# Performance work log

Measured on AMD Instinct MI355X. Metric: run time of the kernel, lower is better.

Reference implementation:

```python
import jax, jax.numpy as jnp
import numpy as np

B, N, DIN, DMID, DOUT, E = 64, 5000, 64, 128, 32, 80000


def setup_inputs() -> dict:
    key = jax.random.key(0)
    ks = jax.random.split(key, 12)
    p = lambda k, shape: jax.random.normal(k, shape, jnp.float32) * 0.05
    return {
        "x": jax.random.normal(ks[0], (B, N, DIN), jnp.float32),
        "edge_index": jax.random.randint(ks[1], (2, E), 0, N),
        "prev_hidden_state": jax.random.normal(ks[2], (B, N, DMID), jnp.float32),
        # GCNConv weights/biases for gates z, r, h
        "Wg_z": p(ks[3], (DIN, DMID)), "bg_z": jnp.zeros((DMID,), jnp.float32),
        "Wg_r": p(ks[4], (DIN, DMID)), "bg_r": jnp.zeros((DMID,), jnp.float32),
        "Wg_h": p(ks[5], (DIN, DMID)), "bg_h": jnp.zeros((DMID,), jnp.float32),
        # gate Linear layers on concat([conv_out, H]) -> DMID
        "Wl_z": p(ks[6], (2 * DMID, DMID)), "bl_z": jnp.zeros((DMID,), jnp.float32),
        "Wl_r": p(ks[7], (2 * DMID, DMID)), "bl_r": jnp.zeros((DMID,), jnp.float32),
        "Wl_h": p(ks[8], (2 * DMID, DMID)), "bl_h": jnp.zeros((DMID,), jnp.float32),
        # final output Linear
        "W_out": p(ks[9], (DMID, DOUT)), "b_out": jnp.zeros((DOUT,), jnp.float32),
    }


def reference(x, edge_index, prev_hidden_state,
              Wg_z, bg_z, Wg_r, bg_r, Wg_h, bg_h,
              Wl_z, bl_z, Wl_r, bl_r, Wl_h, bl_h,
              W_out, b_out):
    # GCN symmetric normalization with self-loops (pyg gcn_norm, improved=False)
    row, col = edge_index[0], edge_index[1]
    loop = jnp.arange(N)
    src = jnp.concatenate([row, loop])          # [E+N]
    dst = jnp.concatenate([col, loop])          # [E+N]
    ew = jnp.ones((E + N,), x.dtype)
    deg = jnp.zeros((N,), x.dtype).at[dst].add(ew)
    dis = jnp.where(deg > 0, jax.lax.rsqrt(jnp.maximum(deg, 1e-12)), 0.0)
    norm = dis[src] * ew * dis[dst]             # [E+N]

    def gcn(w, b):
        xw = jnp.einsum('bnd,de->bne', x, w)            # [B,N,DMID]
        msg = xw[:, src, :] * norm[None, :, None]       # gather + weight
        out = jnp.zeros((B, N, w.shape[1]), x.dtype).at[:, dst, :].add(msg)
        return out + b

    H = prev_hidden_state
    Z = jax.nn.sigmoid(jnp.concatenate([gcn(Wg_z, bg_z), H], -1) @ Wl_z + bl_z)
    R = jax.nn.sigmoid(jnp.concatenate([gcn(Wg_r, bg_r), H], -1) @ Wl_r + bl_r)
    Ht = jnp.tanh(jnp.concatenate([gcn(Wg_h, bg_h), H * R], -1) @ Wl_h + bl_h)
    H_new = Z * H + (1.0 - Z) * Ht                      # [B,N,DMID]

    y = jnp.mean(H_new, axis=1)                         # MeanAggregation over nodes
    y = jax.nn.relu(y) @ W_out + b_out                  # [B,DOUT]
    return (y, H_new)
```

## Files before the change

### kernel.cpp

```cpp
#include <hip/hip_runtime.h>
#include <cmath>

namespace {

constexpr int B = 64, N = 5000, DIN = 64, DMID = 128, DOUT = 32, E = 80000;

typedef unsigned short u16;
typedef __attribute__((ext_vector_type(8))) short short8;
typedef __attribute__((ext_vector_type(4))) float floatx4;

#define MFMA16(a, b, c) __builtin_amdgcn_mfma_f32_16x16x32_bf16((a), (b), (c), 0, 0, 0)

__device__ __forceinline__ u16 f2bf(float f) {
  union { float f; unsigned u; } v; v.f = f;
  unsigned r = v.u + 0x7FFFu + ((v.u >> 16) & 1u);
  return (u16)(r >> 16);
}
__device__ __forceinline__ float bf2f(u16 s) {
  union { unsigned u; float f; } v; v.u = ((unsigned)s) << 16;
  return v.f;
}
__device__ __forceinline__ float sigmoid_fast(float x) {
  return __builtin_amdgcn_rcpf(1.f + __expf(-x));
}
__device__ __forceinline__ float tanh_fast(float x) {
  return fmaf(2.f, __builtin_amdgcn_rcpf(1.f + __expf(-2.f * x)), -1.f);
}


__global__ void zero_kernel(int* counts, int* fill, float* msum) {
  int i = blockIdx.x * 256 + threadIdx.x;
  if (i < N) { counts[i] = 0; fill[i] = 0; }
  if (i < B * DMID) msum[i] = 0.f;
}

__global__ void count_kernel(const int* __restrict__ ei, int* counts) {
  int e = blockIdx.x * 256 + threadIdx.x;
  if (e < E) atomicAdd(&counts[ei[E + e]], 1);
}

__global__ void scan_kernel(const int* __restrict__ counts, int* rowptr, float* dis) {
  __shared__ int sdata[1024];
  const int tid = threadIdx.x;
  constexpr int CH = (N + 1023) / 1024;
  int local[CH];
  int s = 0;
  for (int i = 0; i < CH; i++) {
    int idx = tid * CH + i;
    int c = (idx < N) ? counts[idx] : 0;
    local[i] = s;
    s += c;
  }
  sdata[tid] = s;
  __syncthreads();
  for (int off = 1; off < 1024; off <<= 1) {
    int v = (tid >= off) ? sdata[tid - off] : 0;
    __syncthreads();
    sdata[tid] += v;
    __syncthreads();
  }
  int prev = (tid > 0) ? sdata[tid - 1] : 0;
  for (int i = 0; i < CH; i++) {
    int idx = tid * CH + i;
    if (idx < N) {
      rowptr[idx] = prev + local[i];
      dis[idx] = rsqrtf((float)(counts[idx] + 1));
    }
  }
  if (tid == 1023) rowptr[N] = sdata[1023];
}

__global__ void fill_kernel(const int* __restrict__ ei, const int* __restrict__ rowptr,
                            const float* __restrict__ dis, int* fill,
                            int* csr_src, float* csr_w) {
  int e = blockIdx.x * 256 + threadIdx.x;
  if (e >= E) return;
  int r = ei[e], c = ei[E + e];
  int pos = rowptr[c] + atomicAdd(&fill[c], 1);
  csr_src[pos] = r;
  csr_w[pos] = dis[r] * dis[c];
}


__global__ void pack_kernel(const float* Wgz, const float* Wgr, const float* Wgh,
                            const float* Wlz, const float* Wlr, const float* Wlh,
                            const float* bgz, const float* bgr, const float* bgh,
                            const float* blz, const float* blr, const float* blh,
                            u16* wcB, u16* whB, float* bcAll) {
  int t = blockIdx.x * 256 + threadIdx.x;
  const float* Wg[3] = {Wgz, Wgr, Wgh};
  const float* Wl[3] = {Wlz, Wlr, Wlh};
  const float* bg[3] = {bgz, bgr, bgh};
  const float* bl[3] = {blz, blr, blh};
  if (t < 48 * 64) {
    int chunk = t >> 6, lane = t & 63;
    int q = lane >> 4, lm = lane & 15;
    int g = chunk >> 4, rem = chunk & 15, kt = rem >> 3, nt = rem & 7;
    int n = nt * 16 + lm;
#pragma unroll
    for (int jj = 0; jj < 8; jj++) {
      int k = kt * 32 + q * 8 + jj;
      float acc = 0.f;
      for (int j = 0; j < DMID; j++)
        acc = fmaf(Wg[g][k * DMID + j], Wl[g][j * DMID + n], acc);
      wcB[(size_t)(chunk * 64 + lane) * 8 + jj] = f2bf(acc);
    }
  } else if (t < 48 * 64 + 96 * 64) {
    int t2 = t - 48 * 64;
    int chunk = t2 >> 6, lane = t2 & 63;
    int q = lane >> 4, lm = lane & 15;
    int g = chunk >> 5, rem = chunk & 31, kt = rem >> 3, nt = rem & 7;
    int n = nt * 16 + lm;
#pragma unroll
    for (int jj = 0; jj < 8; jj++) {
      int k = kt * 32 + q * 8 + jj;
      whB[(size_t)t2 * 8 + jj] = f2bf(Wl[g][(DMID + k) * DMID + n]);
    }
  } else {
    int t3 = t - 48 * 64 - 96 * 64;
    if (t3 < 384) {
      int g = t3 >> 7, n = t3 & 127;
      float acc = bl[g][n];
      for (int j = 0; j < DMID; j++)
        acc = fmaf(bg[g][j], Wl[g][j * DMID + n], acc);
      bcAll[t3] = acc;
    }
  }
}


__global__ __launch_bounds__(256) void agg_kernel(
    const float* __restrict__ x, const int* __restrict__ rowptr,
    const int* __restrict__ csr_src, const float* __restrict__ csr_w,
    const float* __restrict__ dis, u16* __restrict__ xs) {
  const int sub = threadIdx.x >> 4;
  const int l16 = threadIdx.x & 15;
  const int unit = blockIdx.x * 16 + sub;
  const int b = unit / N;
  const int n = unit - b * N;
  const float* xb = x + (size_t)b * N * DIN;
  const float d = dis[n];
  float4 v = *(const float4*)(xb + (size_t)n * DIN + l16 * 4);
  const float sw = d * d;
  float ax = v.x * sw, ay = v.y * sw, az = v.z * sw, aw = v.w * sw;
  const int s1 = rowptr[n + 1];
  int p = rowptr[n];
  for (; p + 2 <= s1; p += 2) {
    int i0 = csr_src[p], i1 = csr_src[p + 1];
    float w0 = csr_w[p], w1 = csr_w[p + 1];
    float4 a0 = *(const float4*)(xb + (size_t)i0 * DIN + l16 * 4);
    float4 a1 = *(const float4*)(xb + (size_t)i1 * DIN + l16 * 4);
    ax = fmaf(a0.x, w0, ax); ay = fmaf(a0.y, w0, ay);
    az = fmaf(a0.z, w0, az); aw = fmaf(a0.w, w0, aw);
    ax = fmaf(a1.x, w1, ax); ay = fmaf(a1.y, w1, ay);
    az = fmaf(a1.z, w1, az); aw = fmaf(a1.w, w1, aw);
  }
  if (p < s1) {
    int i0 = csr_src[p];
    float w0 = csr_w[p];
    float4 a0 = *(const float4*)(xb + (size_t)i0 * DIN + l16 * 4);
    ax = fmaf(a0.x, w0, ax); ay = fmaf(a0.y, w0, ay);
    az = fmaf(a0.z, w0, az); aw = fmaf(a0.w, w0, aw);
  }
  uint2 o;
  o.x = (unsigned)f2bf(ax) | ((unsigned)f2bf(ay) << 16);
  o.y = (unsigned)f2bf(az) | ((unsigned)f2bf(aw) << 16);
  *(uint2*)(xs + (size_t)unit * DIN + l16 * 4) = o;
}


constexpr int SH = 136;
constexpr int SX = 72;

__global__ __launch_bounds__(256, 4) void fused_mfma(
    const u16* __restrict__ xs, const float* __restrict__ H,
    const u16* __restrict__ wcB, const u16* __restrict__ whB,
    const float* __restrict__ bcAll,
    float* __restrict__ hnew, float* __restrict__ msum) {
  __shared__ u16 H_s[64 * SH];
  __shared__ u16 XS_s[64 * SX];

  const int tid = threadIdx.x;
  const int b = blockIdx.y;
  const int n0 = blockIdx.x * 64;
  const int lane = tid & 63, w = tid >> 6;
  const int q = lane >> 4, lm = lane & 15;
  const int w16 = w * 16;

#pragma unroll
  for (int i = 0; i < 2; i++) {
    int idx = i * 256 + tid;
    int row = idx >> 3, seg = idx & 7;
    uint4 v = make_uint4(0u, 0u, 0u, 0u);
    if (n0 + row < N) v = *(const uint4*)(xs + ((size_t)b * N + n0 + row) * DIN + seg * 8);
    *(uint4*)&XS_s[row * SX + seg * 8] = v;
  }
#pragma unroll
  for (int i = 0; i < 8; i++) {
    int idx = i * 256 + tid;
    int row = idx >> 5, seg = idx & 31;
    float4 v = make_float4(0.f, 0.f, 0.f, 0.f);
    if (n0 + row < N) v = *(const float4*)(H + ((size_t)b * N + n0 + row) * DMID + seg * 4);
    uint2 p;
    p.x = (unsigned)f2bf(v.x) | ((unsigned)f2bf(v.y) << 16);
    p.y = (unsigned)f2bf(v.z) | ((unsigned)f2bf(v.w) << 16);
    *(uint2*)&H_s[row * SH + seg * 4] = p;
  }
  __syncthreads();

  short8 ax[2], ah[4];
#pragma unroll
  for (int kt = 0; kt < 2; kt++)
    ax[kt] = *(const short8*)&XS_s[(w16 + lm) * SX + kt * 32 + q * 8];
#pragma unroll
  for (int kt = 0; kt < 4; kt++)
    ah[kt] = *(const short8*)&H_s[(w16 + lm) * SH + kt * 32 + q * 8];

  floatx4 racc[8];
#pragma unroll
  for (int nt = 0; nt < 8; nt++) {
    floatx4 a = {0.f, 0.f, 0.f, 0.f};
#pragma unroll
    for (int kt = 0; kt < 2; kt++)
      a = MFMA16(ax[kt], *(const short8*)(wcB + (size_t)((16 + kt * 8 + nt) * 64 + lane) * 8), a);
#pragma unroll
    for (int kt = 0; kt < 4; kt++)
      a = MFMA16(ah[kt], *(const short8*)(whB + (size_t)((32 + kt * 8 + nt) * 64 + lane) * 8), a);
    float bias = bcAll[128 + nt * 16 + lm];
#pragma unroll
    for (int r = 0; r < 4; r++) racc[nt][r] = a[r] + bias;
  }

#pragma unroll
  for (int nt = 0; nt < 8; nt++)
#pragma unroll
    for (int r = 0; r < 4; r++) {
      int row = w16 + q * 4 + r, col = nt * 16 + lm;
      float h = bf2f(H_s[row * SH + col]);
      float rg = sigmoid_fast(racc[nt][r]);
      H_s[row * SH + col] = f2bf(h * rg);
      racc[nt][r] = h;
    }
  __syncthreads();

  short8 ahr[4];
#pragma unroll
  for (int kt = 0; kt < 4; kt++)
    ahr[kt] = *(const short8*)&H_s[(w16 + lm) * SH + kt * 32 + q * 8];

#pragma unroll
  for (int nt = 0; nt < 8; nt++) {
    floatx4 za = {0.f, 0.f, 0.f, 0.f}, ha = {0.f, 0.f, 0.f, 0.f};
#pragma unroll
    for (int kt = 0; kt < 2; kt++) {
      za = MFMA16(ax[kt], *(const short8*)(wcB + (size_t)((0 + kt * 8 + nt) * 64 + lane) * 8), za);
      ha = MFMA16(ax[kt], *(const short8*)(wcB + (size_t)((32 + kt * 8 + nt) * 64 + lane) * 8), ha);
    }
#pragma unroll
    for (int kt = 0; kt < 4; kt++) {
      za = MFMA16(ah[kt], *(const short8*)(whB + (size_t)((0 + kt * 8 + nt) * 64 + lane) * 8), za);
      ha = MFMA16(ahr[kt], *(const short8*)(whB + (size_t)((64 + kt * 8 + nt) * 64 + lane) * 8), ha);
    }
    float zb = bcAll[nt * 16 + lm], hb = bcAll[256 + nt * 16 + lm];
    float colsum = 0.f;
#pragma unroll
    for (int r = 0; r < 4; r++) {
      int row = w16 + q * 4 + r;
      bool valid = (n0 + row) < N;
      float z = sigmoid_fast(za[r] + zb);
      float ht = tanh_fast(ha[r] + hb);
      float h = racc[nt][r];
      float hn = fmaf(z, h - ht, ht);
      if (valid) {
        hnew[((size_t)b * N + n0 + row) * DMID + nt * 16 + lm] = hn;
        colsum += hn;
      }
    }
    colsum += __shfl_xor(colsum, 16);
    colsum += __shfl_xor(colsum, 32);
    if (lane < 16) atomicAdd(&msum[b * DMID + nt * 16 + lane], colsum);
  }
}


__global__ void out_kernel(const float* __restrict__ msum, const float* __restrict__ Wout,
                           const float* __restrict__ bout, float* __restrict__ y) {
  const int b = blockIdx.x;
  const int o = threadIdx.x;
  __shared__ float m[DMID];
  for (int jj = o; jj < DMID; jj += 32)
    m[jj] = fmaxf(msum[b * DMID + jj] * (1.f / (float)N), 0.f);
  __syncthreads();
  float acc = bout[o];
  for (int jj = 0; jj < DMID; jj++)
    acc = fmaf(m[jj], Wout[jj * DOUT + o], acc);
  y[b * DOUT + o] = acc;
}

}

extern "C" void kernel_launch(void* const* d_in, const int* in_sizes, int n_in,
                              void* d_out, int out_size, void* d_ws, size_t ws_size,
                              hipStream_t stream) {
  const float* x = (const float*)d_in[0];
  const int* ei = (const int*)d_in[1];
  const float* H = (const float*)d_in[2];
  const float* Wgz = (const float*)d_in[3];
  const float* bgz = (const float*)d_in[4];
  const float* Wgr = (const float*)d_in[5];
  const float* bgr = (const float*)d_in[6];
  const float* Wgh = (const float*)d_in[7];
  const float* bgh = (const float*)d_in[8];
  const float* Wlz = (const float*)d_in[9];
  const float* blz = (const float*)d_in[10];
  const float* Wlr = (const float*)d_in[11];
  const float* blr = (const float*)d_in[12];
  const float* Wlh = (const float*)d_in[13];
  const float* blh = (const float*)d_in[14];
  const float* Wout = (const float*)d_in[15];
  const float* bout = (const float*)d_in[16];

  float* y = (float*)d_out;
  float* hnew = (float*)d_out + (size_t)B * DOUT;

  char* p = (char*)d_ws;
  auto carve = [&](size_t bytes) {
    char* q = p;
    p += (bytes + 255) & ~size_t(255);
    return q;
  };
  int* counts = (int*)carve((size_t)N * 4);
  int* rowptr = (int*)carve((size_t)(N + 1) * 4);
  int* fill = (int*)carve((size_t)N * 4);
  int* csr_src = (int*)carve((size_t)E * 4);
  float* csr_w = (float*)carve((size_t)E * 4);
  float* dis = (float*)carve((size_t)N * 4);
  float* msum = (float*)carve((size_t)B * DMID * 4);
  u16* wcB = (u16*)carve((size_t)48 * 64 * 8 * 2);
  u16* whB = (u16*)carve((size_t)96 * 64 * 8 * 2);
  float* bcAll = (float*)carve((size_t)384 * 4);
  u16* xs = (u16*)carve((size_t)B * N * DIN * 2);

  zero_kernel<<<(B * DMID + 255) / 256, 256, 0, stream>>>(counts, fill, msum);
  pack_kernel<<<38, 256, 0, stream>>>(Wgz, Wgr, Wgh, Wlz, Wlr, Wlh,
                                      bgz, bgr, bgh, blz, blr, blh,
                                      wcB, whB, bcAll);
  count_kernel<<<(E + 255) / 256, 256, 0, stream>>>(ei, counts);
  scan_kernel<<<1, 1024, 0, stream>>>(counts, rowptr, dis);
  fill_kernel<<<(E + 255) / 256, 256, 0, stream>>>(ei, rowptr, dis, fill, csr_src, csr_w);
  agg_kernel<<<B * N / 16, 256, 0, stream>>>(x, rowptr, csr_src, csr_w, dis, xs);
  fused_mfma<<<dim3((N + 63) / 64, B), 256, 0, stream>>>(xs, H, wcB, whB, bcAll,
                                                         hnew, msum);
  out_kernel<<<B, 32, 0, stream>>>(msum, Wout, bout, y);
}
```

Before: 702.5 us.

## Fuse graph aggregation into MFMA gate kernel and use per-block partial sums

Moves the sparse neighbor aggregation of x directly into the fused MFMA kernel, writing the aggregated bf16 rows straight to shared memory instead of round-tripping a B*N*DIN bf16 buffer through global memory. Replaces global atomics for the node mean with LDS atomics plus a per-block partials array reduced in out_kernel, which also removes the msum zeroing. Occupancy hint is raised to 6 blocks. The trade-off is that irregular gather latency now sits inside the MFMA kernel, may stall its tensor work, and raises register pressure.

```diff
diff --git a/kernel.cpp b/kernel.cpp
--- a/kernel.cpp
+++ b/kernel.cpp
@@ -4,6 +4,7 @@
 namespace {
 
 constexpr int B = 64, N = 5000, DIN = 64, DMID = 128, DOUT = 32, E = 80000;
+constexpr int NT = (N + 63) / 64;
 
 typedef unsigned short u16;
 typedef __attribute__((ext_vector_type(8))) short short8;
@@ -28,10 +29,9 @@
 }
 
 
-__global__ void zero_kernel(int* counts, int* fill, float* msum) {
+__global__ void zero_kernel(int* counts, int* fill) {
   int i = blockIdx.x * 256 + threadIdx.x;
   if (i < N) { counts[i] = 0; fill[i] = 0; }
-  if (i < B * DMID) msum[i] = 0.f;
 }
 
 __global__ void count_kernel(const int* __restrict__ ei, int* counts) {
@@ -129,56 +129,19 @@
 }
 
 
-__global__ __launch_bounds__(256) void agg_kernel(
+constexpr int SH = 136;
+constexpr int SX = 72;
+
+__global__ __launch_bounds__(256, 6) void fused_mfma(
     const float* __restrict__ x, const int* __restrict__ rowptr,
     const int* __restrict__ csr_src, const float* __restrict__ csr_w,
-    const float* __restrict__ dis, u16* __restrict__ xs) {
-  const int sub = threadIdx.x >> 4;
-  const int l16 = threadIdx.x & 15;
-  const int unit = blockIdx.x * 16 + sub;
-  const int b = unit / N;
-  const int n = unit - b * N;
-  const float* xb = x + (size_t)b * N * DIN;
-  const float d = dis[n];
-  float4 v = *(const float4*)(xb + (size_t)n * DIN + l16 * 4);
-  const float sw = d * d;
-  float ax = v.x * sw, ay = v.y * sw, az = v.z * sw, aw = v.w * sw;
-  const int s1 = rowptr[n + 1];
-  int p = rowptr[n];
-  for (; p + 2 <= s1; p += 2) {
-    int i0 = csr_src[p], i1 = csr_src[p + 1];
-    float w0 = csr_w[p], w1 = csr_w[p + 1];
-    float4 a0 = *(const float4*)(xb + (size_t)i0 * DIN + l16 * 4);
-    float4 a1 = *(const float4*)(xb + (size_t)i1 * DIN + l16 * 4);
-    ax = fmaf(a0.x, w0, ax); ay = fmaf(a0.y, w0, ay);
-    az = fmaf(a0.z, w0, az); aw = fmaf(a0.w, w0, aw);
-    ax = fmaf(a1.x, w1, ax); ay = fmaf(a1.y, w1, ay);
-    az = fmaf(a1.z, w1, az); aw = fmaf(a1.w, w1, aw);
-  }
-  if (p < s1) {
-    int i0 = csr_src[p];
-    float w0 = csr_w[p];
-    float4 a0 = *(const float4*)(xb + (size_t)i0 * DIN + l16 * 4);
-    ax = fmaf(a0.x, w0, ax); ay = fmaf(a0.y, w0, ay);
-    az = fmaf(a0.z, w0, az); aw = fmaf(a0.w, w0, aw);
-  }
-  uint2 o;
-  o.x = (unsigned)f2bf(ax) | ((unsigned)f2bf(ay) << 16);
-  o.y = (unsigned)f2bf(az) | ((unsigned)f2bf(aw) << 16);
-  *(uint2*)(xs + (size_t)unit * DIN + l16 * 4) = o;
-}
-
-
-constexpr int SH = 136;
-constexpr int SX = 72;
-
-__global__ __launch_bounds__(256, 4) void fused_mfma(
-    const u16* __restrict__ xs, const float* __restrict__ H,
+    const float* __restrict__ dis, const float* __restrict__ H,
     const u16* __restrict__ wcB, const u16* __restrict__ whB,
     const float* __restrict__ bcAll,
-    float* __restrict__ hnew, float* __restrict__ msum) {
+    float* __restrict__ hnew, float* __restrict__ partials) {
   __shared__ u16 H_s[64 * SH];
   __shared__ u16 XS_s[64 * SX];
+  __shared__ float lds_sum[DMID];
 
   const int tid = threadIdx.x;
   const int b = blockIdx.y;
@@ -187,14 +150,47 @@
   const int q = lane >> 4, lm = lane & 15;
   const int w16 = w * 16;
 
-#pragma unroll
-  for (int i = 0; i < 2; i++) {
-    int idx = i * 256 + tid;
-    int row = idx >> 3, seg = idx & 7;
-    uint4 v = make_uint4(0u, 0u, 0u, 0u);
-    if (n0 + row < N) v = *(const uint4*)(xs + ((size_t)b * N + n0 + row) * DIN + seg * 8);
-    *(uint4*)&XS_s[row * SX + seg * 8] = v;
-  }
+  if (tid < DMID) lds_sum[tid] = 0.f;
+
+  const float* xb = x + (size_t)b * N * DIN;
+  const int l16 = tid & 15;
+  const int u = tid >> 4;
+#pragma unroll
+  for (int pass = 0; pass < 4; pass++) {
+    int row = pass * 16 + u;
+    int n = n0 + row;
+    float ax_ = 0.f, ay_ = 0.f, az_ = 0.f, aw_ = 0.f;
+    if (n < N) {
+      float d = dis[n];
+      float4 v = *(const float4*)(xb + (size_t)n * DIN + l16 * 4);
+      float sw = d * d;
+      ax_ = v.x * sw; ay_ = v.y * sw; az_ = v.z * sw; aw_ = v.w * sw;
+      int p = rowptr[n];
+      const int s1 = rowptr[n + 1];
+      for (; p + 2 <= s1; p += 2) {
+        int i0 = csr_src[p], i1 = csr_src[p + 1];
+        float w0 = csr_w[p], w1 = csr_w[p + 1];
+        float4 a0 = *(const float4*)(xb + (size_t)i0 * DIN + l16 * 4);
+        float4 a1 = *(const float4*)(xb + (size_t)i1 * DIN + l16 * 4);
+        ax_ = fmaf(a0.x, w0, ax_); ay_ = fmaf(a0.y, w0, ay_);
+        az_ = fmaf(a0.z, w0, az_); aw_ = fmaf(a0.w, w0, aw_);
+        ax_ = fmaf(a1.x, w1, ax_); ay_ = fmaf(a1.y, w1, ay_);
+        az_ = fmaf(a1.z, w1, az_); aw_ = fmaf(a1.w, w1, aw_);
+      }
+      if (p < s1) {
+        int i0 = csr_src[p];
+        float w0 = csr_w[p];
+        float4 a0 = *(const float4*)(xb + (size_t)i0 * DIN + l16 * 4);
+        ax_ = fmaf(a0.x, w0, ax_); ay_ = fmaf(a0.y, w0, ay_);
+        az_ = fmaf(a0.z, w0, az_); aw_ = fmaf(a0.w, w0, aw_);
+      }
+    }
+    uint2 o;
+    o.x = (unsigned)f2bf(ax_) | ((unsigned)f2bf(ay_) << 16);
+    o.y = (unsigned)f2bf(az_) | ((unsigned)f2bf(aw_) << 16);
+    *(uint2*)&XS_s[row * SX + l16 * 4] = o;
+  }
+
 #pragma unroll
   for (int i = 0; i < 8; i++) {
     int idx = i * 256 + tid;
@@ -278,23 +274,31 @@
     }
     colsum += __shfl_xor(colsum, 16);
     colsum += __shfl_xor(colsum, 32);
-    if (lane < 16) atomicAdd(&msum[b * DMID + nt * 16 + lane], colsum);
-  }
-}
-
-
-__global__ void out_kernel(const float* __restrict__ msum, const float* __restrict__ Wout,
+    if (lane < 16) atomicAdd(&lds_sum[nt * 16 + lane], colsum);
+  }
+
+  __syncthreads();
+  if (tid < DMID)
+    partials[((size_t)b * NT + blockIdx.x) * DMID + tid] = lds_sum[tid];
+}
+
+
+__global__ void out_kernel(const float* __restrict__ partials, const float* __restrict__ Wout,
                            const float* __restrict__ bout, float* __restrict__ y) {
   const int b = blockIdx.x;
-  const int o = threadIdx.x;
+  const int c = threadIdx.x;
   __shared__ float m[DMID];
-  for (int jj = o; jj < DMID; jj += 32)
-    m[jj] = fmaxf(msum[b * DMID + jj] * (1.f / (float)N), 0.f);
-  __syncthreads();
-  float acc = bout[o];
-  for (int jj = 0; jj < DMID; jj++)
-    acc = fmaf(m[jj], Wout[jj * DOUT + o], acc);
-  y[b * DOUT + o] = acc;
+  float acc = 0.f;
+  for (int t = 0; t < NT; t++)
+    acc += partials[((size_t)b * NT + t) * DMID + c];
+  m[c] = fmaxf(acc * (1.f / (float)N), 0.f);
+  __syncthreads();
+  if (c < DOUT) {
+    float a2 = bout[c];
+    for (int jj = 0; jj < DMID; jj++)
+      a2 = fmaf(m[jj], Wout[jj * DOUT + c], a2);
+    y[b * DOUT + c] = a2;
+  }
 }
 
 }
@@ -335,21 +339,19 @@
   int* csr_src = (int*)carve((size_t)E * 4);
   float* csr_w = (float*)carve((size_t)E * 4);
   float* dis = (float*)carve((size_t)N * 4);
-  float* msum = (float*)carve((size_t)B * DMID * 4);
   u16* wcB = (u16*)carve((size_t)48 * 64 * 8 * 2);
   u16* whB = (u16*)carve((size_t)96 * 64 * 8 * 2);
   float* bcAll = (float*)carve((size_t)384 * 4);
-  u16* xs = (u16*)carve((size_t)B * N * DIN * 2);
-
-  zero_kernel<<<(B * DMID + 255) / 256, 256, 0, stream>>>(counts, fill, msum);
+  float* partials = (float*)carve((size_t)B * NT * DMID * 4);
+
+  zero_kernel<<<(N + 255) / 256, 256, 0, stream>>>(counts, fill);
   pack_kernel<<<38, 256, 0, stream>>>(Wgz, Wgr, Wgh, Wlz, Wlr, Wlh,
                                       bgz, bgr, bgh, blz, blr, blh,
                                       wcB, whB, bcAll);
   count_kernel<<<(E + 255) / 256, 256, 0, stream>>>(ei, counts);
   scan_kernel<<<1, 1024, 0, stream>>>(counts, rowptr, dis);
   fill_kernel<<<(E + 255) / 256, 256, 0, stream>>>(ei, rowptr, dis, fill, csr_src, csr_w);
-  agg_kernel<<<B * N / 16, 256, 0, stream>>>(x, rowptr, csr_src, csr_w, dis, xs);
-  fused_mfma<<<dim3((N + 63) / 64, B), 256, 0, stream>>>(xs, H, wcB, whB, bcAll,
-                                                         hnew, msum);
-  out_kernel<<<B, 32, 0, stream>>>(msum, Wout, bout, y);
-}
+  fused_mfma<<<dim3(NT, B), 256, 0, stream>>>(x, rowptr, csr_src, csr_w, dis, H,
+                                              wcB, whB, bcAll, hnew, partials);
+  out_kernel<<<B, DMID, 0, stream>>>(partials, Wout, bout, y);
+}
```

Result: slower. 961.8 us (+36.9%).
